# Kernel optimization log

Hardware: AMD Instinct MI355X
Metric: run time of the kernel (lower is better)

The kernel has to match this reference:

```python
import jax, jax.numpy as jnp
import numpy as np
import math

D_MODEL = 1024
N_HEADS = 16
HEAD_DIM = D_MODEL // N_HEADS
MLP_DIM = 4 * D_MODEL
B, L, M = 2, 2048, 2048


def layer_norm(x, g, b, eps=1e-5):
    mu = jnp.mean(x, axis=-1, keepdims=True)
    var = jnp.var(x, axis=-1, keepdims=True)
    return (x - mu) * jax.lax.rsqrt(var + eps) * g + b


def mha(q_in, k_in, qW, wW, oW, mask=None):
    # Faithful to source: k and v share w_proj, and the value einsum uses k.
    b, l, _ = q_in.shape
    m = k_in.shape[1]
    q = (q_in @ qW).reshape(b, l, HEAD_DIM, N_HEADS)
    k = (k_in @ wW).reshape(b, m, HEAD_DIM, N_HEADS)
    s = jnp.einsum('bldn,bmdn->blmn', q, k)
    if mask is not None:
        s = jnp.where(mask, -1e9, s)  # mask applied BEFORE scaling, as in source
    s = s / math.sqrt(HEAD_DIM)
    w = jax.nn.softmax(s, axis=2)
    x = jnp.einsum('blmn,bmdn->bldn', w, k)  # source bug: uses k, not v
    x = x.reshape(b, l, HEAD_DIM * N_HEADS)
    return x @ oW


def setup_inputs() -> dict:
    key = jax.random.key(0)
    ks = jax.random.split(key, 16)
    sc = 1.0 / math.sqrt(D_MODEL)
    inp = {
        'x': jax.random.normal(ks[0], (B, L, D_MODEL), jnp.float32),
        'enc_output': jax.random.normal(ks[1], (B, M, D_MODEL), jnp.float32),
        'mask': jax.random.randint(ks[2], (B, 1, M, 1), 0, 2).astype(bool),
        'q1W': jax.random.normal(ks[3], (D_MODEL, D_MODEL), jnp.float32) * sc,
        'w1W': jax.random.normal(ks[4], (D_MODEL, D_MODEL), jnp.float32) * sc,
        'o1W': jax.random.normal(ks[5], (D_MODEL, D_MODEL), jnp.float32) * sc,
        'q2W': jax.random.normal(ks[6], (D_MODEL, D_MODEL), jnp.float32) * sc,
        'w2W': jax.random.normal(ks[7], (D_MODEL, D_MODEL), jnp.float32) * sc,
        'o2W': jax.random.normal(ks[8], (D_MODEL, D_MODEL), jnp.float32) * sc,
        'ffW1': jax.random.normal(ks[9], (D_MODEL, MLP_DIM), jnp.float32) * sc,
        'ffb1': jnp.zeros((MLP_DIM,), jnp.float32),
        'ffW2': jax.random.normal(ks[10], (MLP_DIM, D_MODEL), jnp.float32) * sc,
        'ffb2': jnp.zeros((D_MODEL,), jnp.float32),
        'g1': jnp.ones((D_MODEL,), jnp.float32), 'b1': jnp.zeros((D_MODEL,), jnp.float32),
        'g2': jnp.ones((D_MODEL,), jnp.float32), 'b2': jnp.zeros((D_MODEL,), jnp.float32),
        'g3': jnp.ones((D_MODEL,), jnp.float32), 'b3': jnp.zeros((D_MODEL,), jnp.float32),
    }
    return inp


def reference(x, enc_output, mask, q1W, w1W, o1W, q2W, w2W, o2W,
              ffW1, ffb1, ffW2, ffb2, g1, b1, g2, b2, g3, b3):
    # self-attention (no mask, as in source)
    sa = mha(x, x, q1W, w1W, o1W, mask=None)
    x = layer_norm(x + sa, g1, b1)
    # encoder-decoder attention with mask
    ca = mha(x, enc_output, q2W, w2W, o2W, mask=mask)
    x = layer_norm(x + ca, g2, b2)
    # feed-forward (exact GELU, matching torch nn.GELU default)
    h = jax.nn.gelu(x @ ffW1 + ffb1, approximate=False)
    ff = h @ ffW2 + ffb2
    x = layer_norm(x + ff, g3, b3)
    return x
```

## Files before the change

### kernel.cpp

```cpp
#include <hip/hip_runtime.h>
#include <hip/hip_bf16.h>
#include <math.h>
#include <stdint.h>

typedef __attribute__((ext_vector_type(8))) short bf16x8_t;
typedef __attribute__((ext_vector_type(4))) float f32x4_t;

#define LOG2E 1.4426950408889634f
#define GLB(p) ((const __attribute__((address_space(1))) void*)(p))
#define LDS(p) ((__attribute__((address_space(3))) void*)(p))

__device__ __forceinline__ unsigned short f2bf(float f) {
    union { float f; unsigned int u; } v; v.f = f;
    unsigned int r = v.u + 0x7FFFu + ((v.u >> 16) & 1u);
    return (unsigned short)(r >> 16);
}

__device__ __forceinline__ float bf2f(unsigned short us) {
    union { unsigned int u; float f; } c; c.u = (unsigned int)us << 16; return c.f;
}

__device__ __forceinline__ unsigned int pack2bf(float a, float b) {
#if __has_builtin(__builtin_amdgcn_cvt_pk_bf16_f32)
    auto r = __builtin_amdgcn_cvt_pk_bf16_f32(a, b);
    unsigned int u;
    __builtin_memcpy(&u, &r, 4);
    return u;
#else
    return (unsigned int)f2bf(a) | ((unsigned int)f2bf(b) << 16);
#endif
}

__device__ __forceinline__ float fast_rcp(float x) {
#if __has_builtin(__builtin_amdgcn_rcpf)
    return __builtin_amdgcn_rcpf(x);
#else
    return 1.0f / x;
#endif
}

__device__ __forceinline__ float gelu_fast(float v) {
    float x2 = v * v;
    float inner = v * fmaf(0.0356774081f, x2, 0.7978845608f);
    inner = fminf(fmaxf(inner, -20.f), 20.f);
    float t = exp2f(inner * 2.8853900817779268f);
    return v * t * fast_rcp(t + 1.0f);
}

__global__ void cast2_bf16_k(const float* __restrict__ inA, unsigned short* __restrict__ outA,
                             const float* __restrict__ inB, unsigned short* __restrict__ outB,
                             int n4, const int* __restrict__ maskp, float* __restrict__ mask4) {
    if (blockIdx.y == 2) {
        int i = blockIdx.x * blockDim.x + threadIdx.x;
        if (i < 8192) {
            int nt = i & 3, l16 = (i >> 2) & 15, t = (i >> 6) & 31, b = (i >> 11) & 1;
            mask4[i] = maskp[b * 2048 + t * 64 + nt * 16 + l16] ? -1e10f : 0.0f;
        }
        return;
    }
    const float* in = blockIdx.y ? inB : inA;
    unsigned short* out = blockIdx.y ? outB : outA;
    int i = blockIdx.x * blockDim.x + threadIdx.x;
    if (i < n4) {
        float4 v = ((const float4*)in)[i];
        ushort4 o;
        o.x = f2bf(v.x); o.y = f2bf(v.y); o.z = f2bf(v.z); o.w = f2bf(v.w);
        ((ushort4*)out)[i] = o;
    }
}

__global__ void transpose_all_k(const float* __restrict__ s0, const float* __restrict__ s1,
                                const float* __restrict__ s2, const float* __restrict__ s3,
                                const float* __restrict__ s4, const float* __restrict__ s5,
                                const float* __restrict__ s6, const float* __restrict__ s7,
                                unsigned short* __restrict__ d0, unsigned short* __restrict__ d1,
                                unsigned short* __restrict__ d2, unsigned short* __restrict__ d3,
                                unsigned short* __restrict__ d4, unsigned short* __restrict__ d5,
                                unsigned short* __restrict__ d6, unsigned short* __restrict__ d7) {
    __shared__ float tile[32][33];
    int idx = blockIdx.x;
    const float* W; unsigned short* Wt; int K, N, bx, by;
    if (idx < 6144) {
        int which = idx >> 10, t = idx & 1023;
        bx = t & 31; by = t >> 5; K = 1024; N = 1024;
        switch (which) {
            case 0: W = s0; Wt = d0; break;
            case 1: W = s1; Wt = d1; break;
            case 2: W = s2; Wt = d2; break;
            case 3: W = s3; Wt = d3; break;
            case 4: W = s4; Wt = d4; break;
            default: W = s5; Wt = d5; break;
        }
    } else if (idx < 10240) {
        int t = idx - 6144;
        bx = t & 127; by = t >> 7; K = 1024; N = 4096;
        W = s6; Wt = d6;
    } else {
        int t = idx - 10240;
        bx = t & 31; by = t >> 5; K = 4096; N = 1024;
        W = s7; Wt = d7;
    }
    int k0 = by * 32, n0 = bx * 32;
    int tx = threadIdx.x, ty = threadIdx.y;
#pragma unroll
    for (int i = 0; i < 32; i += 8)
        tile[ty + i][tx] = W[(long)(k0 + ty + i) * N + n0 + tx];
    __syncthreads();
#pragma unroll
    for (int i = 0; i < 32; i += 8)
        Wt[(long)(n0 + ty + i) * K + k0 + tx] = f2bf(tile[tx][ty + i]);
}

__global__ __launch_bounds__(256) void split_qk_k(const unsigned short* __restrict__ inQ,
                                                  const unsigned short* __restrict__ inK,
                                                  int stride, int koff,
                                                  unsigned short* __restrict__ Qout,
                                                  unsigned short* __restrict__ Kout) {
    __shared__ __align__(16) unsigned short t[16][1024];
    long l0 = (long)blockIdx.x * 16;
    int tid = threadIdx.x;
    int h = tid >> 4, lr = tid & 15;
    long l = l0 + lr;
    int b = (int)(l >> 11);
    int ll = (int)(l & 2047);
    int sw = ll & 7;

    for (int c = tid; c < 2048; c += 256) {
        int r = c >> 7, col = (c & 127) * 8;
        *(uint4*)(&t[r][col]) = *(const uint4*)(inQ + (l0 + r) * stride + col);
    }
    __syncthreads();
    {
        unsigned short* op = Qout + ((long)(b * 16 + h) * 2048 + ll) * 64;
#pragma unroll
        for (int g = 0; g < 8; g++) {
            union { uint4 v; unsigned short s[8]; } u;
#pragma unroll
            for (int j = 0; j < 8; j++) u.s[j] = t[lr][(g * 8 + j) * 16 + h];
            *(uint4*)(op + (g ^ sw) * 8) = u.v;
        }
    }
    __syncthreads();
    for (int c = tid; c < 2048; c += 256) {
        int r = c >> 7, col = (c & 127) * 8;
        *(uint4*)(&t[r][col]) = *(const uint4*)(inK + (l0 + r) * stride + koff + col);
    }
    __syncthreads();
    {
        unsigned short* op = Kout + ((long)(b * 16 + h) * 2048 + ll) * 64;
#pragma unroll
        for (int g = 0; g < 8; g++) {
            union { uint4 v; unsigned short s[8]; } u;
#pragma unroll
            for (int j = 0; j < 8; j++) u.s[j] = t[lr][(g * 8 + j) * 16 + h];
            *(uint4*)(op + (g ^ sw) * 8) = u.v;
        }
    }
}

__global__ __launch_bounds__(256) void transpose_heads_perm_k(const unsigned short* __restrict__ in,
                                                              unsigned short* __restrict__ out) {
    __shared__ unsigned short t[64][72];
    int bh = blockIdx.y;
    int m0 = blockIdx.x * 64;
    int tid = threadIdx.x;
    for (int c = tid; c < 512; c += 256) {
        int r = c >> 3, gp = c & 7;
        int glog = gp ^ (r & 7);
        uint4 v = *(const uint4*)(in + ((long)bh * 2048 + m0 + r) * 64 + gp * 8);
        *(uint4*)(&t[r][glog * 8]) = v;
    }
    __syncthreads();
    for (int c = tid; c < 512; c += 256) {
        int d = c >> 3, pb = (c & 7) * 8;
        union { uint4 v; unsigned short s[8]; } u;
#pragma unroll
        for (int j = 0; j < 8; j++) {
            int p = pb + j;
            int m = (p >> 2) + (p & 3) * 16;
            u.s[j] = t[m][d];
        }
        int gph = (pb >> 3) ^ (d & 7);
        *(uint4*)(out + ((long)bh * 64 + d) * 2048 + m0 + gph * 8) = u.v;
    }
}

template <int EP, int BN>
__global__ __launch_bounds__(256) void gemm_k(const unsigned short* __restrict__ A,
                                              const unsigned short* __restrict__ Bt,
                                              void* __restrict__ outp,
                                              const float* __restrict__ bias,
                                              const unsigned short* __restrict__ A2,
                                              const unsigned short* __restrict__ Bt2,
                                              void* __restrict__ out2,
                                              int M, int N, int K) {
    if (blockIdx.z) { A = A2; Bt = Bt2; outp = out2; }
    __shared__ __align__(16) unsigned short As[128 * 64];
    __shared__ __align__(16) unsigned short Bs[BN * 64];
    const int NT = BN / 32;
    const int BG = BN / 32;
    int tid = threadIdx.x;
    int wave = tid >> 6, lane = tid & 63;
    int wm = wave >> 1, wn = wave & 1;
    int quad = lane >> 4, l16 = lane & 15;
    int bm = blockIdx.y * 128, bn = blockIdx.x * BN;

    f32x4_t acc[4][NT] = {};

    int srow = tid >> 3;
    int sgrp = (tid & 7) ^ (srow & 7);
    const unsigned short* Ag[4];
#pragma unroll
    for (int i = 0; i < 4; i++)
        Ag[i] = A + (long)(bm + i * 32 + srow) * K + sgrp * 8;
    const unsigned short* Bg[BG];
#pragma unroll
    for (int i = 0; i < BG; i++)
        Bg[i] = Bt + (long)(bn + i * 32 + srow) * K + sgrp * 8;

    for (int k0 = 0; k0 < K; k0 += 64) {
        __syncthreads();
#pragma unroll
        for (int i = 0; i < 4; i++)
            __builtin_amdgcn_global_load_lds(GLB(Ag[i] + k0), LDS(As + i * 2048 + tid * 8), 16, 0, 0);
#pragma unroll
        for (int i = 0; i < BG; i++)
            __builtin_amdgcn_global_load_lds(GLB(Bg[i] + k0), LDS(Bs + i * 2048 + tid * 8), 16, 0, 0);
        __syncthreads();
#pragma unroll
        for (int kk = 0; kk < 2; kk++) {
            int xg = ((kk * 4 + quad) ^ (l16 & 7)) * 8;
            bf16x8_t af[4], bfr[NT];
#pragma unroll
            for (int t = 0; t < 4; t++)
                af[t] = *(const bf16x8_t*)(As + (wm * 64 + t * 16 + l16) * 64 + xg);
#pragma unroll
            for (int t = 0; t < NT; t++)
                bfr[t] = *(const bf16x8_t*)(Bs + (wn * (BN / 2) + t * 16 + l16) * 64 + xg);
#pragma unroll
            for (int mt = 0; mt < 4; mt++)
#pragma unroll
                for (int nt = 0; nt < NT; nt++)
                    acc[mt][nt] = __builtin_amdgcn_mfma_f32_16x16x32_bf16(af[mt], bfr[nt], acc[mt][nt], 0, 0, 0);
        }
    }

#pragma unroll
    for (int mt = 0; mt < 4; mt++)
#pragma unroll
        for (int nt = 0; nt < NT; nt++)
#pragma unroll
            for (int r = 0; r < 4; r++) {
                int gm = bm + wm * 64 + mt * 16 + quad * 4 + r;
                int gn = bn + wn * (BN / 2) + nt * 16 + l16;
                float v = acc[mt][nt][r];
                if (EP == 0) {
                    ((float*)outp)[(long)gm * N + gn] = v;
                } else if (EP == 2) {
                    v = gelu_fast(v + bias[gn]);
                    ((unsigned short*)outp)[(long)gm * N + gn] = f2bf(v);
                } else if (EP == 3) {
                    ((float*)outp)[(long)gm * N + gn] = v + bias[gn];
                } else if (EP == 6) {
                    ((unsigned short*)outp)[(long)gm * N + gn] = f2bf(v + bias[gn]);
                } else {
                    ((unsigned short*)outp)[(long)gm * N + gn] = f2bf(v);
                }
            }
}

template <int USE_MASK>
__global__ __launch_bounds__(256, 4) void flash_attn8_k(const unsigned short* __restrict__ Qh,
                                                        const unsigned short* __restrict__ Kh,
                                                        const unsigned short* __restrict__ KhTp,
                                                        const float* __restrict__ mask4,
                                                        unsigned short* __restrict__ out) {
    __shared__ __align__(16) unsigned short K1[2 * 64 * 64];
    __shared__ __align__(16) unsigned short K2[2 * 64 * 64];
    __shared__ __align__(16) unsigned short Ps[64 * 64];
    __shared__ __align__(16) float Ml[USE_MASK ? 2048 : 4];

    int tid = threadIdx.x;
    int wave = tid >> 6, lane = tid & 63;
    int quad = lane >> 4, l16 = lane & 15;
    int bh = blockIdx.y, b = bh >> 4, h = bh & 15;
    int l0 = blockIdx.x * 64;
    const unsigned short* k1p = Kh + (long)bh * 2048 * 64 + tid * 8;
    const unsigned short* k2p = KhTp + (long)bh * 64 * 2048 + (long)(tid >> 3) * 2048 + (tid & 7) * 8;

    int sw = l16 & 7;

    const unsigned short* qrow = Qh + ((long)bh * 2048 + l0 + wave * 16 + l16) * 64;
    bf16x8_t qf[2];
#pragma unroll
    for (int kk = 0; kk < 2; kk++)
        qf[kk] = *(const bf16x8_t*)(qrow + ((kk * 4 + quad) ^ sw) * 8);

    if (USE_MASK) {
        const float* mp = mask4 + b * 2048;
        for (int c = tid; c < 512; c += 256)
            ((float4*)Ml)[c] = ((const float4*)mp)[c];
    }
    __syncthreads();

#define STAGE_KV(buf)                                                                                   \
    do {                                                                                                \
        __builtin_amdgcn_global_load_lds(GLB(k1p), LDS(K1 + (buf) * 4096 + tid * 8), 16, 0, 0);         \
        __builtin_amdgcn_global_load_lds(GLB(k1p + 2048), LDS(K1 + (buf) * 4096 + tid * 8 + 2048), 16, 0, 0); \
        __builtin_amdgcn_global_load_lds(GLB(k2p), LDS(K2 + (buf) * 4096 + tid * 8), 16, 0, 0);         \
        __builtin_amdgcn_global_load_lds(GLB(k2p + 32 * 2048), LDS(K2 + (buf) * 4096 + tid * 8 + 2048), 16, 0, 0); \
    } while (0)

    STAGE_KV(0);

    const float C1 = 0.125f * LOG2E;
    f32x4_t acc_o[4] = {};
    float rs[4] = {0.f, 0.f, 0.f, 0.f};

    for (int t = 0; t < 32; ++t) {
        int cur = t & 1;
        if (t < 31) {
            k1p += 4096;
            k2p += 64;
            STAGE_KV(cur ^ 1);
            asm volatile("s_waitcnt vmcnt(4)\n\ts_barrier" ::: "memory");
        } else {
            asm volatile("s_waitcnt vmcnt(0)\n\ts_barrier" ::: "memory");
        }
        const unsigned short* K1c = K1 + (cur << 12);
        const unsigned short* K2c = K2 + (cur << 12);

        float4 mq = make_float4(0.f, 0.f, 0.f, 0.f);
        if (USE_MASK) mq = *(const float4*)(Ml + t * 64 + l16 * 4);

        f32x4_t sacc[4] = {};
        __builtin_amdgcn_s_setprio(1);
#pragma unroll
        for (int kk = 0; kk < 2; kk++) {
            int xg = ((kk * 4 + quad) ^ sw) * 8;
#pragma unroll
            for (int nt = 0; nt < 4; nt++) {
                bf16x8_t bfr = *(const bf16x8_t*)(K1c + (nt * 16 + l16) * 64 + xg);
                sacc[nt] = __builtin_amdgcn_mfma_f32_16x16x32_bf16(qf[kk], bfr, sacc[nt], 0, 0, 0);
            }
        }
        __builtin_amdgcn_s_setprio(0);

#pragma unroll
        for (int r = 0; r < 4; r++) {
            float p0 = exp2f(fmaf(sacc[0][r], C1, mq.x));
            float p1 = exp2f(fmaf(sacc[1][r], C1, mq.y));
            float p2 = exp2f(fmaf(sacc[2][r], C1, mq.z));
            float p3 = exp2f(fmaf(sacc[3][r], C1, mq.w));
            rs[r] += (p0 + p1) + (p2 + p3);
            uint2 pk; pk.x = pack2bf(p0, p1); pk.y = pack2bf(p2, p3);
            int Rrow = wave * 16 + quad * 4 + r;
            int grp = (l16 >> 1) ^ (Rrow & 7);
            *(uint2*)(Ps + Rrow * 64 + grp * 8 + (l16 & 1) * 4) = pk;
        }

        __builtin_amdgcn_s_setprio(1);
#pragma unroll
        for (int kk = 0; kk < 2; kk++) {
            int xg = ((kk * 4 + quad) ^ sw) * 8;
            int Rr = wave * 16 + l16;
            int pg = ((kk * 4 + quad) ^ (l16 & 7)) * 8;
            bf16x8_t af = *(const bf16x8_t*)(Ps + Rr * 64 + pg);
#pragma unroll
            for (int nt = 0; nt < 4; nt++) {
                bf16x8_t bfr = *(const bf16x8_t*)(K2c + (nt * 16 + l16) * 64 + xg);
                acc_o[nt] = __builtin_amdgcn_mfma_f32_16x16x32_bf16(af, bfr, acc_o[nt], 0, 0, 0);
            }
        }
        __builtin_amdgcn_s_setprio(0);

        asm volatile("s_barrier" ::: "memory");
    }
#undef STAGE_KV

#pragma unroll
    for (int r = 0; r < 4; r++) {
#pragma unroll
        for (int d = 1; d < 16; d <<= 1) rs[r] += __shfl_xor(rs[r], d);
    }

#pragma unroll
    for (int r = 0; r < 4; r++) {
        float inv = 1.0f / rs[r];
        int l = l0 + wave * 16 + quad * 4 + r;
#pragma unroll
        for (int nt = 0; nt < 4; nt++) {
            int d = nt * 16 + l16;
            out[((long)(b * 2048 + l)) * 1024 + d * 16 + h] = f2bf(acc_o[nt][r] * inv);
        }
    }
}

template <int AIN_BF16, int OUT_F32>
__global__ __launch_bounds__(256) void resid_ln_k(const void* __restrict__ ap,
                                                  const unsigned short* __restrict__ rb,
                                                  const float* __restrict__ g,
                                                  const float* __restrict__ bb,
                                                  float* __restrict__ outf,
                                                  unsigned short* __restrict__ outb) {
    long row = blockIdx.x;
    int tid = threadIdx.x;
    float x0, x1, x2, x3;
    if (AIN_BF16) {
        ushort4 va = ((const ushort4*)((const unsigned short*)ap + row * 1024))[tid];
        x0 = bf2f(va.x); x1 = bf2f(va.y); x2 = bf2f(va.z); x3 = bf2f(va.w);
    } else {
        float4 va = ((const float4*)((const float*)ap + row * 1024))[tid];
        x0 = va.x; x1 = va.y; x2 = va.z; x3 = va.w;
    }
    ushort4 vr = ((const ushort4*)(rb + row * 1024))[tid];
    x0 += bf2f(vr.x); x1 += bf2f(vr.y); x2 += bf2f(vr.z); x3 += bf2f(vr.w);
    float s = x0 + x1 + x2 + x3;
    float sq = x0 * x0 + x1 * x1 + x2 * x2 + x3 * x3;
#pragma unroll
    for (int d = 1; d < 64; d <<= 1) { s += __shfl_xor(s, d); sq += __shfl_xor(sq, d); }
    __shared__ float ss[4], ssq[4];
    int wave = tid >> 6, lane = tid & 63;
    if (lane == 0) { ss[wave] = s; ssq[wave] = sq; }
    __syncthreads();
    s = ss[0] + ss[1] + ss[2] + ss[3];
    sq = ssq[0] + ssq[1] + ssq[2] + ssq[3];
    float mean = s * (1.0f / 1024.0f);
    float var = sq * (1.0f / 1024.0f) - mean * mean;
    float rstd = rsqrtf(var + 1e-5f);
    float4 vg = ((const float4*)g)[tid];
    float4 vb = ((const float4*)bb)[tid];
    float y0 = (x0 - mean) * rstd * vg.x + vb.x;
    float y1 = (x1 - mean) * rstd * vg.y + vb.y;
    float y2 = (x2 - mean) * rstd * vg.z + vb.z;
    float y3 = (x3 - mean) * rstd * vg.w + vb.w;
    if (OUT_F32) {
        float4 o; o.x = y0; o.y = y1; o.z = y2; o.w = y3;
        ((float4*)(outf + row * 1024))[tid] = o;
    } else {
        ushort4 ob; ob.x = f2bf(y0); ob.y = f2bf(y1); ob.z = f2bf(y2); ob.w = f2bf(y3);
        ((ushort4*)(outb + row * 1024))[tid] = ob;
    }
}

extern "C" void kernel_launch(void* const* d_in, const int* in_sizes, int n_in,
                              void* d_out, int out_size, void* d_ws, size_t ws_size,
                              hipStream_t stream) {
    const float* x    = (const float*)d_in[0];
    const float* enc  = (const float*)d_in[1];
    const int*   mask = (const int*)d_in[2];
    const float* q1W  = (const float*)d_in[3];
    const float* w1W  = (const float*)d_in[4];
    const float* o1W  = (const float*)d_in[5];
    const float* q2W  = (const float*)d_in[6];
    const float* w2W  = (const float*)d_in[7];
    const float* o2W  = (const float*)d_in[8];
    const float* ffW1 = (const float*)d_in[9];
    const float* ffb1 = (const float*)d_in[10];
    const float* ffW2 = (const float*)d_in[11];
    const float* ffb2 = (const float*)d_in[12];
    const float* g1 = (const float*)d_in[13];
    const float* b1 = (const float*)d_in[14];
    const float* g2 = (const float*)d_in[15];
    const float* b2 = (const float*)d_in[16];
    const float* g3 = (const float*)d_in[17];
    const float* b3 = (const float*)d_in[18];
    float* outp = (float*)d_out;

    const int T = 4096;
    const int D = 1024;
    const int F = 4096;

    char* ws = (char*)d_ws;
    auto alloc = [&](size_t sz) { char* p = ws; ws += (sz + 255) & ~(size_t)255; return p; };
    unsigned short* qw1Wt = (unsigned short*)alloc((size_t)2 * D * D * 2);
    unsigned short* o1Wt  = (unsigned short*)alloc((size_t)D * D * 2);
    unsigned short* q2Wt  = (unsigned short*)alloc((size_t)D * D * 2);
    unsigned short* w2Wt  = (unsigned short*)alloc((size_t)D * D * 2);
    unsigned short* o2Wt  = (unsigned short*)alloc((size_t)D * D * 2);
    unsigned short* ffW1t = (unsigned short*)alloc((size_t)F * D * 2);
    unsigned short* ffW2t = (unsigned short*)alloc((size_t)D * F * 2);
    unsigned short* xb    = (unsigned short*)alloc((size_t)T * D * 2);
    unsigned short* encb  = (unsigned short*)alloc((size_t)T * D * 2);
    unsigned short* Qhb   = (unsigned short*)alloc((size_t)T * D * 2);
    unsigned short* Khb   = (unsigned short*)alloc((size_t)T * D * 2);
    unsigned short* KhTb  = (unsigned short*)alloc((size_t)T * D * 2);
    unsigned short* attnb = (unsigned short*)alloc((size_t)T * D * 2);
    float*          mask4b= (float*)alloc((size_t)8192 * 4);
    unsigned short* projb = (unsigned short*)alloc((size_t)T * D * 2);
    unsigned short* x1s   = (unsigned short*)alloc((size_t)T * D * 2);
    unsigned short* x2s   = (unsigned short*)alloc((size_t)T * D * 2);
    unsigned short* S1    = (unsigned short*)alloc((size_t)T * F * 2);
    unsigned short* tmpqw = S1;
    unsigned short* q2o   = S1;
    unsigned short* w2o   = S1 + (size_t)T * D;
    unsigned short* hb    = S1;

    dim3 blk256(256);
    dim3 tblk(32, 8);

    cast2_bf16_k<<<dim3(T * D / 4 / 256, 3), blk256, 0, stream>>>(x, xb, enc, encb, T * D / 4, mask, mask4b);
    transpose_all_k<<<dim3(14336), tblk, 0, stream>>>(
        q1W, w1W, o1W, q2W, w2W, o2W, ffW1, ffW2,
        qw1Wt, qw1Wt + (size_t)D * D, o1Wt, q2Wt, w2Wt, o2Wt, ffW1t, ffW2t);

    gemm_k<4, 64><<<dim3(2 * D / 64, T / 128, 1), blk256, 0, stream>>>(
        xb, qw1Wt, tmpqw, nullptr, nullptr, nullptr, nullptr, T, 2 * D, D);
    split_qk_k<<<dim3(T / 16), blk256, 0, stream>>>(tmpqw, tmpqw, 2 * D, D, Qhb, Khb);
    transpose_heads_perm_k<<<dim3(32, 32), blk256, 0, stream>>>(Khb, KhTb);
    flash_attn8_k<0><<<dim3(32, 32), blk256, 0, stream>>>(Qhb, Khb, KhTb, nullptr, attnb);
    gemm_k<4, 64><<<dim3(D / 64, T / 128, 1), blk256, 0, stream>>>(
        attnb, o1Wt, projb, nullptr, nullptr, nullptr, nullptr, T, D, D);
    resid_ln_k<0, 0><<<dim3(T), blk256, 0, stream>>>(x, projb, g1, b1, nullptr, x1s);

    gemm_k<4, 64><<<dim3(D / 64, T / 128, 2), blk256, 0, stream>>>(
        x1s, q2Wt, q2o, nullptr, encb, w2Wt, w2o, T, D, D);
    split_qk_k<<<dim3(T / 16), blk256, 0, stream>>>(q2o, w2o, D, 0, Qhb, Khb);
    transpose_heads_perm_k<<<dim3(32, 32), blk256, 0, stream>>>(Khb, KhTb);
    flash_attn8_k<1><<<dim3(32, 32), blk256, 0, stream>>>(Qhb, Khb, KhTb, mask4b, attnb);
    gemm_k<4, 64><<<dim3(D / 64, T / 128, 1), blk256, 0, stream>>>(
        attnb, o2Wt, projb, nullptr, nullptr, nullptr, nullptr, T, D, D);
    resid_ln_k<1, 0><<<dim3(T), blk256, 0, stream>>>(x1s, projb, g2, b2, nullptr, x2s);

    gemm_k<2, 128><<<dim3(F / 128, T / 128, 1), blk256, 0, stream>>>(
        x2s, ffW1t, hb, ffb1, nullptr, nullptr, nullptr, T, F, D);
    gemm_k<6, 64><<<dim3(D / 64, T / 128, 1), blk256, 0, stream>>>(
        hb, ffW2t, projb, ffb2, nullptr, nullptr, nullptr, T, D, F);
    resid_ln_k<1, 1><<<dim3(T), blk256, 0, stream>>>(x2s, projb, g3, b3, outp, nullptr);
}
```

Before: 585.8 us.

## Triple-buffer GEMM K-loop with async LDS loads and bit-pack attention mask

Adds a PIPE=3 path to the GEMM kernel that keeps three LDS stages of A/B tiles in flight. It waits with explicit vmcnt counts so global-to-LDS loads overlap MFMA compute, and applies this to the output-projection and FFN2 GEMMs. The attention mask is also packed into 32-bit words per lane, replacing the float mask table staged in shared memory with per-tile bit tests. This raises LDS usage per block and relies on hand-written vmcnt literals that assume BN=64.

```diff
diff --git a/kernel.cpp b/kernel.cpp
--- a/kernel.cpp
+++ b/kernel.cpp
@@ -49,12 +49,15 @@
 
 __global__ void cast2_bf16_k(const float* __restrict__ inA, unsigned short* __restrict__ outA,
                              const float* __restrict__ inB, unsigned short* __restrict__ outB,
-                             int n4, const int* __restrict__ maskp, float* __restrict__ mask4) {
+                             int n4, const int* __restrict__ maskp, unsigned int* __restrict__ maskbits) {
     if (blockIdx.y == 2) {
         int i = blockIdx.x * blockDim.x + threadIdx.x;
-        if (i < 8192) {
-            int nt = i & 3, l16 = (i >> 2) & 15, t = (i >> 6) & 31, b = (i >> 11) & 1;
-            mask4[i] = maskp[b * 2048 + t * 64 + nt * 16 + l16] ? -1e10f : 0.0f;
+        if (i < 128) {
+            int nt = i & 3, l16 = (i >> 2) & 15, b = i >> 6;
+            unsigned int w = 0;
+            for (int t = 0; t < 32; t++)
+                w |= (maskp[b * 2048 + t * 64 + nt * 16 + l16] ? 1u : 0u) << t;
+            maskbits[i] = w;
         }
         return;
     }
@@ -185,7 +188,7 @@
     }
 }
 
-template <int EP, int BN>
+template <int EP, int BN, int PIPE>
 __global__ __launch_bounds__(256) void gemm_k(const unsigned short* __restrict__ A,
                                               const unsigned short* __restrict__ Bt,
                                               void* __restrict__ outp,
@@ -194,9 +197,10 @@
                                               const unsigned short* __restrict__ Bt2,
                                               void* __restrict__ out2,
                                               int M, int N, int K) {
+    static_assert(BN == 64 || PIPE == 1, "vmcnt literals assume BN==64 in PIPE=3 path");
     if (blockIdx.z) { A = A2; Bt = Bt2; outp = out2; }
-    __shared__ __align__(16) unsigned short As[128 * 64];
-    __shared__ __align__(16) unsigned short Bs[BN * 64];
+    __shared__ __align__(16) unsigned short As[PIPE * 128 * 64];
+    __shared__ __align__(16) unsigned short Bs[PIPE * BN * 64];
     const int NT = BN / 32;
     const int BG = BN / 32;
     int tid = threadIdx.x;
@@ -218,30 +222,58 @@
     for (int i = 0; i < BG; i++)
         Bg[i] = Bt + (long)(bn + i * 32 + srow) * K + sgrp * 8;
 
-    for (int k0 = 0; k0 < K; k0 += 64) {
-        __syncthreads();
+    auto stage = [&](int buf, int k0) {
 #pragma unroll
         for (int i = 0; i < 4; i++)
-            __builtin_amdgcn_global_load_lds(GLB(Ag[i] + k0), LDS(As + i * 2048 + tid * 8), 16, 0, 0);
+            __builtin_amdgcn_global_load_lds(GLB(Ag[i] + k0), LDS(As + buf * 8192 + i * 2048 + tid * 8), 16, 0, 0);
 #pragma unroll
         for (int i = 0; i < BG; i++)
-            __builtin_amdgcn_global_load_lds(GLB(Bg[i] + k0), LDS(Bs + i * 2048 + tid * 8), 16, 0, 0);
-        __syncthreads();
+            __builtin_amdgcn_global_load_lds(GLB(Bg[i] + k0), LDS(Bs + buf * (BN * 64) + i * 2048 + tid * 8), 16, 0, 0);
+    };
+
+    auto compute = [&](int buf) {
+        const unsigned short* Ab = As + buf * 8192;
+        const unsigned short* Bb = Bs + buf * (BN * 64);
 #pragma unroll
         for (int kk = 0; kk < 2; kk++) {
             int xg = ((kk * 4 + quad) ^ (l16 & 7)) * 8;
             bf16x8_t af[4], bfr[NT];
 #pragma unroll
             for (int t = 0; t < 4; t++)
-                af[t] = *(const bf16x8_t*)(As + (wm * 64 + t * 16 + l16) * 64 + xg);
+                af[t] = *(const bf16x8_t*)(Ab + (wm * 64 + t * 16 + l16) * 64 + xg);
 #pragma unroll
             for (int t = 0; t < NT; t++)
-                bfr[t] = *(const bf16x8_t*)(Bs + (wn * (BN / 2) + t * 16 + l16) * 64 + xg);
+                bfr[t] = *(const bf16x8_t*)(Bb + (wn * (BN / 2) + t * 16 + l16) * 64 + xg);
 #pragma unroll
             for (int mt = 0; mt < 4; mt++)
 #pragma unroll
                 for (int nt = 0; nt < NT; nt++)
                     acc[mt][nt] = __builtin_amdgcn_mfma_f32_16x16x32_bf16(af[mt], bfr[nt], acc[mt][nt], 0, 0, 0);
+        }
+    };
+
+    if (PIPE == 3) {
+        stage(0, 0);
+        stage(1, 64);
+        const int NS = K >> 6;
+        for (int i = 0; i < NS; i++) {
+            if (i + 2 < NS) {
+                stage((i + 2) % 3, (i + 2) * 64);
+                asm volatile("s_waitcnt vmcnt(12)\n\ts_barrier" ::: "memory");
+            } else if (i + 1 < NS) {
+                asm volatile("s_waitcnt vmcnt(6)\n\ts_barrier" ::: "memory");
+            } else {
+                asm volatile("s_waitcnt vmcnt(0)\n\ts_barrier" ::: "memory");
+            }
+            compute(i % 3);
+            asm volatile("s_barrier" ::: "memory");
+        }
+    } else {
+        for (int k0 = 0; k0 < K; k0 += 64) {
+            __syncthreads();
+            stage(0, k0);
+            __syncthreads();
+            compute(0);
         }
     }
 
@@ -270,15 +302,14 @@
 }
 
 template <int USE_MASK>
-__global__ __launch_bounds__(256, 4) void flash_attn8_k(const unsigned short* __restrict__ Qh,
-                                                        const unsigned short* __restrict__ Kh,
-                                                        const unsigned short* __restrict__ KhTp,
-                                                        const float* __restrict__ mask4,
-                                                        unsigned short* __restrict__ out) {
+__global__ __launch_bounds__(256, 4) void flash_attn10_k(const unsigned short* __restrict__ Qh,
+                                                         const unsigned short* __restrict__ Kh,
+                                                         const unsigned short* __restrict__ KhTp,
+                                                         const unsigned int* __restrict__ maskbits,
+                                                         unsigned short* __restrict__ out) {
     __shared__ __align__(16) unsigned short K1[2 * 64 * 64];
     __shared__ __align__(16) unsigned short K2[2 * 64 * 64];
     __shared__ __align__(16) unsigned short Ps[64 * 64];
-    __shared__ __align__(16) float Ml[USE_MASK ? 2048 : 4];
 
     int tid = threadIdx.x;
     int wave = tid >> 6, lane = tid & 63;
@@ -296,12 +327,8 @@
     for (int kk = 0; kk < 2; kk++)
         qf[kk] = *(const bf16x8_t*)(qrow + ((kk * 4 + quad) ^ sw) * 8);
 
-    if (USE_MASK) {
-        const float* mp = mask4 + b * 2048;
-        for (int c = tid; c < 512; c += 256)
-            ((float4*)Ml)[c] = ((const float4*)mp)[c];
-    }
-    __syncthreads();
+    uint4 mb = make_uint4(0, 0, 0, 0);
+    if (USE_MASK) mb = *(const uint4*)(maskbits + (b * 16 + l16) * 4);
 
 #define STAGE_KV(buf)                                                                                   \
     do {                                                                                                \
@@ -312,6 +339,7 @@
     } while (0)
 
     STAGE_KV(0);
+    __syncthreads();
 
     const float C1 = 0.125f * LOG2E;
     f32x4_t acc_o[4] = {};
@@ -330,8 +358,14 @@
         const unsigned short* K1c = K1 + (cur << 12);
         const unsigned short* K2c = K2 + (cur << 12);
 
-        float4 mq = make_float4(0.f, 0.f, 0.f, 0.f);
-        if (USE_MASK) mq = *(const float4*)(Ml + t * 64 + l16 * 4);
+        float mqx = 0.f, mqy = 0.f, mqz = 0.f, mqw = 0.f;
+        if (USE_MASK) {
+            unsigned int bit = 1u << t;
+            mqx = (mb.x & bit) ? -1e10f : 0.0f;
+            mqy = (mb.y & bit) ? -1e10f : 0.0f;
+            mqz = (mb.z & bit) ? -1e10f : 0.0f;
+            mqw = (mb.w & bit) ? -1e10f : 0.0f;
+        }
 
         f32x4_t sacc[4] = {};
         __builtin_amdgcn_s_setprio(1);
@@ -348,10 +382,10 @@
 
 #pragma unroll
         for (int r = 0; r < 4; r++) {
-            float p0 = exp2f(fmaf(sacc[0][r], C1, mq.x));
-            float p1 = exp2f(fmaf(sacc[1][r], C1, mq.y));
-            float p2 = exp2f(fmaf(sacc[2][r], C1, mq.z));
-            float p3 = exp2f(fmaf(sacc[3][r], C1, mq.w));
+            float p0 = exp2f(fmaf(sacc[0][r], C1, mqx));
+            float p1 = exp2f(fmaf(sacc[1][r], C1, mqy));
+            float p2 = exp2f(fmaf(sacc[2][r], C1, mqz));
+            float p3 = exp2f(fmaf(sacc[3][r], C1, mqw));
             rs[r] += (p0 + p1) + (p2 + p3);
             uint2 pk; pk.x = pack2bf(p0, p1); pk.y = pack2bf(p2, p3);
             int Rrow = wave * 16 + quad * 4 + r;
@@ -486,7 +520,7 @@
     unsigned short* Khb   = (unsigned short*)alloc((size_t)T * D * 2);
     unsigned short* KhTb  = (unsigned short*)alloc((size_t)T * D * 2);
     unsigned short* attnb = (unsigned short*)alloc((size_t)T * D * 2);
-    float*          mask4b= (float*)alloc((size_t)8192 * 4);
+    unsigned int*   maskbb= (unsigned int*)alloc((size_t)128 * 4);
     unsigned short* projb = (unsigned short*)alloc((size_t)T * D * 2);
     unsigned short* x1s   = (unsigned short*)alloc((size_t)T * D * 2);
     unsigned short* x2s   = (unsigned short*)alloc((size_t)T * D * 2);
@@ -499,32 +533,32 @@
     dim3 blk256(256);
     dim3 tblk(32, 8);
 
-    cast2_bf16_k<<<dim3(T * D / 4 / 256, 3), blk256, 0, stream>>>(x, xb, enc, encb, T * D / 4, mask, mask4b);
+    cast2_bf16_k<<<dim3(T * D / 4 / 256, 3), blk256, 0, stream>>>(x, xb, enc, encb, T * D / 4, mask, maskbb);
     transpose_all_k<<<dim3(14336), tblk, 0, stream>>>(
         q1W, w1W, o1W, q2W, w2W, o2W, ffW1, ffW2,
         qw1Wt, qw1Wt + (size_t)D * D, o1Wt, q2Wt, w2Wt, o2Wt, ffW1t, ffW2t);
 
-    gemm_k<4, 64><<<dim3(2 * D / 64, T / 128, 1), blk256, 0, stream>>>(
+    gemm_k<4, 64, 1><<<dim3(2 * D / 64, T / 128, 1), blk256, 0, stream>>>(
         xb, qw1Wt, tmpqw, nullptr, nullptr, nullptr, nullptr, T, 2 * D, D);
     split_qk_k<<<dim3(T / 16), blk256, 0, stream>>>(tmpqw, tmpqw, 2 * D, D, Qhb, Khb);
     transpose_heads_perm_k<<<dim3(32, 32), blk256, 0, stream>>>(Khb, KhTb);
-    flash_attn8_k<0><<<dim3(32, 32), blk256, 0, stream>>>(Qhb, Khb, KhTb, nullptr, attnb);
-    gemm_k<4, 64><<<dim3(D / 64, T / 128, 1), blk256, 0, stream>>>(
+    flash_attn10_k<0><<<dim3(32, 32), blk256, 0, stream>>>(Qhb, Khb, KhTb, nullptr, attnb);
+    gemm_k<4, 64, 3><<<dim3(D / 64, T / 128, 1), blk256, 0, stream>>>(
         attnb, o1Wt, projb, nullptr, nullptr, nullptr, nullptr, T, D, D);
     resid_ln_k<0, 0><<<dim3(T), blk256, 0, stream>>>(x, projb, g1, b1, nullptr, x1s);
 
-    gemm_k<4, 64><<<dim3(D / 64, T / 128, 2), blk256, 0, stream>>>(
+    gemm_k<4, 64, 1><<<dim3(D / 64, T / 128, 2), blk256, 0, stream>>>(
         x1s, q2Wt, q2o, nullptr, encb, w2Wt, w2o, T, D, D);
     split_qk_k<<<dim3(T / 16), blk256, 0, stream>>>(q2o, w2o, D, 0, Qhb, Khb);
     transpose_heads_perm_k<<<dim3(32, 32), blk256, 0, stream>>>(Khb, KhTb);
-    flash_attn8_k<1><<<dim3(32, 32), blk256, 0, stream>>>(Qhb, Khb, KhTb, mask4b, attnb);
-    gemm_k<4, 64><<<dim3(D / 64, T / 128, 1), blk256, 0, stream>>>(
+    flash_attn10_k<1><<<dim3(32, 32), blk256, 0, stream>>>(Qhb, Khb, KhTb, maskbb, attnb);
+    gemm_k<4, 64, 3><<<dim3(D / 64, T / 128, 1), blk256, 0, stream>>>(
         attnb, o2Wt, projb, nullptr, nullptr, nullptr, nullptr, T, D, D);
     resid_ln_k<1, 0><<<dim3(T), blk256, 0, stream>>>(x1s, projb, g2, b2, nullptr, x2s);
 
-    gemm_k<2, 128><<<dim3(F / 128, T / 128, 1), blk256, 0, stream>>>(
+    gemm_k<2, 128, 1><<<dim3(F / 128, T / 128, 1), blk256, 0, stream>>>(
         x2s, ffW1t, hb, ffb1, nullptr, nullptr, nullptr, T, F, D);
-    gemm_k<6, 64><<<dim3(D / 64, T / 128, 1), blk256, 0, stream>>>(
+    gemm_k<6, 64, 3><<<dim3(D / 64, T / 128, 1), blk256, 0, stream>>>(
         hb, ffW2t, projb, ffb2, nullptr, nullptr, nullptr, T, D, F);
     resid_ln_k<1, 1><<<dim3(T), blk256, 0, stream>>>(x2s, projb, g3, b3, outp, nullptr);
 }
```

Result: slower. 602.9 us (+2.9%).
